# Kernel optimization log

Hardware: AMD Instinct MI355X
Metric: run time of the kernel (lower is better)

## Reference

```python
import math
import jax, jax.numpy as jnp
import numpy as np
from jax import lax

_S = 1.0 / (2.0 * math.sqrt(2.0))  # each tap is (1/2)/sqrt(2)


def _haar(x, axis, high, same):
    """2-tap Haar cross-correlation along `axis`.
    low  = [ 1/2, 1/2]/sqrt(2) -> _S*(a+b)
    high = [-1/2, 1/2]/sqrt(2) -> _S*(b-a)
    same=True replicates torch's even-kernel padding='same': one zero on the RIGHT.
    same=False is valid conv (output length n-1).
    """
    if same:
        pad = [(0, 0)] * x.ndim
        pad[axis] = (0, 1)
        x = jnp.pad(x, pad)
    n = x.shape[axis]
    a = lax.slice_in_dim(x, 0, n - 1, axis=axis)
    b = lax.slice_in_dim(x, 1, n, axis=axis)
    return _S * (b - a) if high else _S * (a + b)


def setup_inputs() -> dict:
    key = jax.random.key(0)
    x = jax.random.normal(key, (2, 3, 16, 256, 256), dtype=jnp.float32)
    return {"x": x}


def reference(x):
    # frames axis (dim 2): padding=0 (valid) in the original -> length f-1
    L = _haar(x, 2, False, False)
    H = _haar(x, 2, True, False)
    # height axis (dim 3): padding='same' (zero on right)
    LL = _haar(L, 3, False, True)
    LH = _haar(L, 3, True, True)
    HL = _haar(H, 3, False, True)
    HH = _haar(H, 3, True, True)
    # width axis (dim 4): padding='same'
    LLL = _haar(LL, 4, False, True)
    LLH = _haar(LL, 4, True, True)
    LHL = _haar(LH, 4, False, True)
    LHH = _haar(LH, 4, True, True)
    HLL = _haar(HL, 4, False, True)
    HLH = _haar(HL, 4, True, True)
    HHL = _haar(HH, 4, False, True)
    HHH = _haar(HH, 4, True, True)
    detail = jnp.concatenate((LLH, LHL, LHH, HLL, HLH, HHL, HHH), axis=2)
    # torch .squeeze(1): only drops channel dim if it is size 1
    if detail.shape[1] == 1:
        detail = jnp.squeeze(detail, axis=1)
    return (LLL, detail)
```

## Files before the change

### kernel.cpp

```cpp
#include <hip/hip_runtime.h>
#include <stdint.h>


static constexpr float S = 0.35355339059327373f;
static constexpr int   PLANE = 256 * 256;
static constexpr size_t LLL_ELEMS = (size_t)6 * 15 * PLANE;

__device__ __forceinline__ float4 pack_lo(const float* A) {
    return make_float4(S * (A[0] + A[1]), S * (A[1] + A[2]),
                       S * (A[2] + A[3]), S * (A[3] + A[4]));
}

__device__ __forceinline__ float4 pack_hi(const float* A) {
    return make_float4(S * (A[1] - A[0]), S * (A[2] - A[1]),
                       S * (A[3] - A[2]), S * (A[4] - A[3]));
}

__global__ __launch_bounds__(256) void haar3d_kernel(const float* __restrict__ x,
                                                     float* __restrict__ out) {
    const int tid  = blockIdx.x * 256 + threadIdx.x;
    const int lane = threadIdx.x & 63;
    const int row  = tid >> 6;
    const int h    = row & 255;
    const int t    = row >> 8;
    const int f    = t % 15;
    const int nc   = t / 15;
    const int w    = lane << 2;

    const float* p00 = x + ((size_t)(nc * 16 + f) * 256 + h) * 256 + w;
    const float4 z4 = make_float4(0.f, 0.f, 0.f, 0.f);
    float4 v00 = *(const float4*)(p00);
    float4 v10 = *(const float4*)(p00 + PLANE);
    float4 v01 = z4, v11 = z4;
    if (h < 255) {
        v01 = *(const float4*)(p00 + 256);
        v11 = *(const float4*)(p00 + PLANE + 256);
    }

    const float x00[4] = {v00.x, v00.y, v00.z, v00.w};
    const float x10[4] = {v10.x, v10.y, v10.z, v10.w};
    const float x01[4] = {v01.x, v01.y, v01.z, v01.w};
    const float x11[4] = {v11.x, v11.y, v11.z, v11.w};

    float LL[5], LH[5], HL[5], HH[5];
#pragma unroll
    for (int j = 0; j < 4; ++j) {
        const float l0 = S * (x00[j] + x10[j]);
        const float l1 = S * (x01[j] + x11[j]);
        const float g0 = S * (x10[j] - x00[j]);
        const float g1 = S * (x11[j] - x01[j]);
        LL[j] = S * (l0 + l1);
        LH[j] = S * (l1 - l0);
        HL[j] = S * (g0 + g1);
        HH[j] = S * (g1 - g0);
    }

    const float nLL = __shfl_down(LL[0], 1);
    const float nLH = __shfl_down(LH[0], 1);
    const float nHL = __shfl_down(HL[0], 1);
    const float nHH = __shfl_down(HH[0], 1);
    const bool last = (lane == 63);
    LL[4] = last ? 0.f : nLL;
    LH[4] = last ? 0.f : nLH;
    HL[4] = last ? 0.f : nHL;
    HH[4] = last ? 0.f : nHH;

    const size_t rowOff = ((size_t)h) * 256 + w;
    float* lllDst = out + ((size_t)(nc * 15 + f)) * PLANE + rowOff;
    *(float4*)lllDst = pack_lo(LL);

    float* dbase = out + LLL_ELEMS +
                   ((size_t)nc * 105 + f) * PLANE + rowOff;
    const size_t kStride = (size_t)15 * PLANE;
    *(float4*)(dbase + 0 * kStride) = pack_hi(LL);
    *(float4*)(dbase + 1 * kStride) = pack_lo(LH);
    *(float4*)(dbase + 2 * kStride) = pack_hi(LH);
    *(float4*)(dbase + 3 * kStride) = pack_lo(HL);
    *(float4*)(dbase + 4 * kStride) = pack_hi(HL);
    *(float4*)(dbase + 5 * kStride) = pack_lo(HH);
    *(float4*)(dbase + 6 * kStride) = pack_hi(HH);
}

extern "C" void kernel_launch(void* const* d_in, const int* in_sizes, int n_in,
                              void* d_out, int out_size, void* d_ws, size_t ws_size,
                              hipStream_t stream) {
    const float* x = (const float*)d_in[0];
    float* out = (float*)d_out;
    haar3d_kernel<<<dim3(5760), dim3(256), 0, stream>>>(x, out);
}
```

Measured before the change: 201.7 us.

## Split work by subband per block, 4 rows per thread, nontemporal stores

Each block now computes a single one of the 8 subbands for 16 rows of one frame pair. Each thread loads 5 rows from two frames and writes 4 output rows of that one subband with nontemporal float4 stores, and a block-index swizzle interleaves subbands across launch order. The aim is to give every block a single contiguous output stream instead of eight scattered ones and to avoid polluting the cache with the large output. In exchange the input is re-read up to 8 times, once per subband, and relies on cache hits to keep that cheap.

```diff
diff --git a/kernel.cpp b/kernel.cpp
--- a/kernel.cpp
+++ b/kernel.cpp
@@ -6,79 +6,95 @@
 static constexpr int   PLANE = 256 * 256;
 static constexpr size_t LLL_ELEMS = (size_t)6 * 15 * PLANE;
 
-__device__ __forceinline__ float4 pack_lo(const float* A) {
-    return make_float4(S * (A[0] + A[1]), S * (A[1] + A[2]),
-                       S * (A[2] + A[3]), S * (A[3] + A[4]));
+typedef float f32x4 __attribute__((ext_vector_type(4)));
+
+__device__ __forceinline__ void nt_store(float* p, f32x4 v) {
+    __builtin_nontemporal_store(v, (f32x4*)p);
 }
 
-__device__ __forceinline__ float4 pack_hi(const float* A) {
-    return make_float4(S * (A[1] - A[0]), S * (A[2] - A[1]),
-                       S * (A[3] - A[2]), S * (A[4] - A[3]));
-}
+__global__ __launch_bounds__(256) void haar3d_sub_kernel(const float* __restrict__ x,
+                                                         float* __restrict__ out) {
+    const int bid0 = blockIdx.x;
+    const int bid  = (bid0 & 7) * 1440 + (bid0 >> 3);
 
-__global__ __launch_bounds__(256) void haar3d_kernel(const float* __restrict__ x,
-                                                     float* __restrict__ out) {
-    const int tid  = blockIdx.x * 256 + threadIdx.x;
+    const int k  = bid / 1440;
+    int rem = bid - k * 1440;
+    const int nc = rem / 240;
+    rem -= nc * 240;
+    const int f  = rem >> 4;
+    const int hb = rem & 15;
+    const int wv = threadIdx.x >> 6;
     const int lane = threadIdx.x & 63;
-    const int row  = tid >> 6;
-    const int h    = row & 255;
-    const int t    = row >> 8;
-    const int f    = t % 15;
-    const int nc   = t / 15;
-    const int w    = lane << 2;
+    const int h  = ((hb << 2) + wv) << 2;
+    const int w  = lane << 2;
 
-    const float* p00 = x + ((size_t)(nc * 16 + f) * 256 + h) * 256 + w;
-    const float4 z4 = make_float4(0.f, 0.f, 0.f, 0.f);
-    float4 v00 = *(const float4*)(p00);
-    float4 v10 = *(const float4*)(p00 + PLANE);
-    float4 v01 = z4, v11 = z4;
-    if (h < 255) {
-        v01 = *(const float4*)(p00 + 256);
-        v11 = *(const float4*)(p00 + PLANE + 256);
+    const bool F  = (k >> 2) & 1;
+    const bool Hs = (k >> 1) & 1;
+    const bool W  = k & 1;
+
+    const float* p0 = x + ((size_t)(nc * 16 + f) * 256 + h) * 256 + w;
+    const float* p1 = p0 + PLANE;
+
+    f32x4 a[5], b[5];
+#pragma unroll
+    for (int r = 0; r < 4; ++r) {
+        a[r] = *(const f32x4*)(p0 + r * 256);
+        b[r] = *(const f32x4*)(p1 + r * 256);
+    }
+    if (h < 252) {
+        a[4] = *(const f32x4*)(p0 + 4 * 256);
+        b[4] = *(const f32x4*)(p1 + 4 * 256);
+    } else {
+        a[4] = (f32x4)0.f;
+        b[4] = (f32x4)0.f;
     }
 
-    const float x00[4] = {v00.x, v00.y, v00.z, v00.w};
-    const float x10[4] = {v10.x, v10.y, v10.z, v10.w};
-    const float x01[4] = {v01.x, v01.y, v01.z, v01.w};
-    const float x11[4] = {v11.x, v11.y, v11.z, v11.w};
-
-    float LL[5], LH[5], HL[5], HH[5];
+    float u[4][5];
 #pragma unroll
     for (int j = 0; j < 4; ++j) {
-        const float l0 = S * (x00[j] + x10[j]);
-        const float l1 = S * (x01[j] + x11[j]);
-        const float g0 = S * (x10[j] - x00[j]);
-        const float g1 = S * (x11[j] - x01[j]);
-        LL[j] = S * (l0 + l1);
-        LH[j] = S * (l1 - l0);
-        HL[j] = S * (g0 + g1);
-        HH[j] = S * (g1 - g0);
+        float t[5];
+#pragma unroll
+        for (int r = 0; r < 5; ++r) {
+            const float av = a[r][j];
+            const float bv = b[r][j];
+            t[r] = F ? S * (bv - av) : S * (av + bv);
+        }
+#pragma unroll
+        for (int q = 0; q < 4; ++q)
+            u[q][j] = Hs ? S * (t[q + 1] - t[q]) : S * (t[q] + t[q + 1]);
     }
 
-    const float nLL = __shfl_down(LL[0], 1);
-    const float nLH = __shfl_down(LH[0], 1);
-    const float nHL = __shfl_down(HL[0], 1);
-    const float nHH = __shfl_down(HH[0], 1);
     const bool last = (lane == 63);
-    LL[4] = last ? 0.f : nLL;
-    LH[4] = last ? 0.f : nLH;
-    HL[4] = last ? 0.f : nHL;
-    HH[4] = last ? 0.f : nHH;
+#pragma unroll
+    for (int q = 0; q < 4; ++q) {
+        const float n = __shfl_down(u[q][0], 1);
+        u[q][4] = last ? 0.f : n;
+    }
 
-    const size_t rowOff = ((size_t)h) * 256 + w;
-    float* lllDst = out + ((size_t)(nc * 15 + f)) * PLANE + rowOff;
-    *(float4*)lllDst = pack_lo(LL);
-
-    float* dbase = out + LLL_ELEMS +
-                   ((size_t)nc * 105 + f) * PLANE + rowOff;
-    const size_t kStride = (size_t)15 * PLANE;
-    *(float4*)(dbase + 0 * kStride) = pack_hi(LL);
-    *(float4*)(dbase + 1 * kStride) = pack_lo(LH);
-    *(float4*)(dbase + 2 * kStride) = pack_hi(LH);
-    *(float4*)(dbase + 3 * kStride) = pack_lo(HL);
-    *(float4*)(dbase + 4 * kStride) = pack_hi(HL);
-    *(float4*)(dbase + 5 * kStride) = pack_lo(HH);
-    *(float4*)(dbase + 6 * kStride) = pack_hi(HH);
+    float* dst;
+    if (k == 0) {
+        dst = out + ((size_t)(nc * 15 + f)) * PLANE + (size_t)h * 256 + w;
+    } else {
+        dst = out + LLL_ELEMS +
+              ((size_t)nc * 105 + (size_t)(k - 1) * 15 + f) * PLANE +
+              (size_t)h * 256 + w;
+    }
+#pragma unroll
+    for (int q = 0; q < 4; ++q) {
+        f32x4 o;
+        if (W) {
+            o.x = S * (u[q][1] - u[q][0]);
+            o.y = S * (u[q][2] - u[q][1]);
+            o.z = S * (u[q][3] - u[q][2]);
+            o.w = S * (u[q][4] - u[q][3]);
+        } else {
+            o.x = S * (u[q][0] + u[q][1]);
+            o.y = S * (u[q][1] + u[q][2]);
+            o.z = S * (u[q][2] + u[q][3]);
+            o.w = S * (u[q][3] + u[q][4]);
+        }
+        nt_store(dst + q * 256, o);
+    }
 }
 
 extern "C" void kernel_launch(void* const* d_in, const int* in_sizes, int n_in,
@@ -86,5 +102,5 @@
                               hipStream_t stream) {
     const float* x = (const float*)d_in[0];
     float* out = (float*)d_out;
-    haar3d_kernel<<<dim3(5760), dim3(256), 0, stream>>>(x, out);
+    haar3d_sub_kernel<<<dim3(11520), dim3(256), 0, stream>>>(x, out);
 }
```

After: 226.7 us. 12.4% more time.
